# Optimization experiments

Hardware: AMD Instinct MI355X
Metric: run time of the kernel (lower is better)

The kernel has to match this reference:

```python
import jax, jax.numpy as jnp
import numpy as np

PIANO_SAMPLES = 2_621_440          # multiple of 256 (~119 s @ 22050 Hz)
BLOCK = 512
HOP = 256
N_STEPS = PIANO_SAMPLES // HOP      # 10240 loop iterations
N_FRAMES = PIANO_SAMPLES // HOP + 2 # 10242
UPSAMPLE = 256 // 32                # 8, as in F.upsample(scale_factor=8)


def _hamming(n=BLOCK):
    # torch.hamming_window default: periodic=True
    return (0.54 - 0.46 * jnp.cos(2.0 * jnp.pi * jnp.arange(n, dtype=jnp.float32) / n)).astype(jnp.float32)


def _upsample_linear(v, scale):
    # F.upsample(mode='linear', align_corners=False) on a 1D signal
    n = v.shape[0]
    coords = (jnp.arange(n * scale, dtype=jnp.float32) + 0.5) / scale - 0.5
    coords = jnp.clip(coords, 0.0, n - 1.0)
    lo = jnp.floor(coords).astype(jnp.int32)
    hi = jnp.minimum(lo + 1, n - 1)
    w = coords - lo.astype(jnp.float32)
    return v[lo] * (1.0 - w) + v[hi] * w


def setup_inputs() -> dict:
    key = jax.random.key(0)
    k1, k2, k3, k4, k5, k6 = jax.random.split(key, 6)
    return {
        "x": jnp.zeros((1,), jnp.float32),  # unused by the original forward
        "excitation_env": jax.random.uniform(k1, (N_FRAMES * 32,), jnp.float32) * 0.01,
        "tf_real": jax.random.uniform(k2, (N_FRAMES, 257), jnp.float32) * 0.2,
        "tf_imag": jax.random.uniform(k3, (N_FRAMES, 257), jnp.float32) * 0.2,
        "etf_real": jax.random.uniform(k4, (257,), jnp.float32) * 0.2,
        "etf_imag": jax.random.uniform(k5, (257,), jnp.float32) * 0.2,
        # per-step uniform(-1,1) noise (torch draws this inside forward)
        "noise": jax.random.uniform(k6, (N_STEPS, BLOCK), jnp.float32) * 2.0 - 1.0,
    }


def reference(x, excitation_env, tf_real, tf_imag, etf_real, etf_imag, noise):
    tf = (tf_real + 1j * tf_imag).astype(jnp.complex64)      # [N_FRAMES, 257]
    etf = (etf_real + 1j * etf_imag).astype(jnp.complex64)   # [257]
    win = _hamming()

    # excitation envelope: square then linear-upsample x8 -> len PIANO_SAMPLES + 512
    exc = _upsample_linear(excitation_env ** 2, UPSAMPLE)

    # gather all 512-sample excitation windows at hop 256 -> [N_STEPS, 512]
    idx = jnp.arange(N_STEPS)[:, None] * HOP + jnp.arange(BLOCK)[None, :]
    exc_blocks = exc[idx]

    # batched excitation filtering (independent per step -> fully vectorized)
    imp = noise * exc_blocks
    imp = jnp.fft.irfft(jnp.fft.rfft(imp, norm='ortho') * etf, norm='ortho').astype(jnp.float32)

    # impulse added to the *previous* block at steps 1..N_STEPS-1; last block gets none
    imp_next = jnp.concatenate([imp[1:], jnp.zeros((1, BLOCK), imp.dtype)], axis=0)

    def step(s, inp):
        tf_i, inext = inp
        b = win * jnp.fft.irfft(jnp.fft.rfft(s, norm='ortho') * tf_i, norm='ortho').astype(jnp.float32)
        s_next = b + inext
        return s_next, s_next

    s0 = imp[0]  # learned_impulse=False -> first block is the filtered excitation
    _, ys = jax.lax.scan(step, s0, (tf[:N_STEPS], imp_next))

    blocks = jnp.concatenate([s0[None, :], ys], axis=0)  # [N_STEPS+1, 512]

    # overlap-add with hop 256
    n_b = blocks.shape[0]
    out = jnp.zeros((n_b * HOP + (BLOCK - HOP),), blocks.dtype)
    oa_idx = jnp.arange(n_b)[:, None] * HOP + jnp.arange(BLOCK)[None, :]
    out = out.at[oa_idx].add(blocks)
    return out[:PIANO_SAMPLES]
```

## Files before the change

### kernel.cpp

```cpp
#include <hip/hip_runtime.h>
#include <math.h>

#define N_STEPS 10240
#define ROWF2 264
#define ROWF  (ROWF2*2)
#define SROWF 512
#define ENV_N 327744
#define LCH 16
#define KWARM 16

typedef float f4 __attribute__((ext_vector_type(4)));

__device__ inline float2 mkf2(float x, float y) { return make_float2(x, y); }

template<int DIR>
__device__ inline void waveFFT256(float2 v[4], const int l,
                                  const float Tc, const float Ts,
                                  const float ux, const float uy) {
  const int rb = (int)(__brev((unsigned)l) >> 26);
  #pragma unroll
  for (int r = 0; r < 4; ++r) {
    v[r].x = __shfl(v[r].x, rb);
    v[r].y = __shfl(v[r].y, rb);
  }
  #pragma unroll
  for (int s = 0; s < 6; ++s) {
    const int half = 1 << s;
    float wx, wy;
    if (s == 0) { wx = (l & 1) ? -1.f : 1.f; wy = 0.f; }
    else {
      const int idx = (l << (5 - s)) & 63;
      wx = __shfl(Tc, idx);
      float tsv = __shfl(Ts, idx);
      wy = (DIR < 0) ? tsv : -tsv;
    }
    #pragma unroll
    for (int r = 0; r < 4; ++r) {
      float tx = __shfl_xor(v[r].x, half);
      float ty = __shfl_xor(v[r].y, half);
      const bool low = (l & half) == 0;
      float ax = low ? v[r].x : tx, ay = low ? v[r].y : ty;
      float bx = low ? tx : v[r].x, by = low ? ty : v[r].y;
      v[r].x = ax + (wx * bx - wy * by);
      v[r].y = ay + (wx * by + wy * bx);
    }
  }
  const float u2x = ux * ux - uy * uy, u2y = 2.f * ux * uy;
  const float u3x = u2x * ux - u2y * uy, u3y = u2x * uy + u2y * ux;
  float2 t0 = v[0];
  float2 t1 = mkf2(v[1].x * ux - v[1].y * uy, v[1].x * uy + v[1].y * ux);
  float2 t2 = mkf2(v[2].x * u2x - v[2].y * u2y, v[2].x * u2y + v[2].y * u2x);
  float2 t3 = mkf2(v[3].x * u3x - v[3].y * u3y, v[3].x * u3y + v[3].y * u3x);
  float2 p02 = mkf2(t0.x + t2.x, t0.y + t2.y), m02 = mkf2(t0.x - t2.x, t0.y - t2.y);
  float2 p13 = mkf2(t1.x + t3.x, t1.y + t3.y), m13 = mkf2(t1.x - t3.x, t1.y - t3.y);
  v[0] = mkf2(p02.x + p13.x, p02.y + p13.y);
  v[2] = mkf2(p02.x - p13.x, p02.y - p13.y);
  if (DIR < 0) {
    v[1] = mkf2(m02.x + m13.y, m02.y - m13.x);
    v[3] = mkf2(m02.x - m13.y, m02.y + m13.x);
  } else {
    v[1] = mkf2(m02.x - m13.y, m02.y + m13.x);
    v[3] = mkf2(m02.x + m13.y, m02.y - m13.x);
  }
}

__global__ __launch_bounds__(256) void kernA(const float* __restrict__ env,
                                             const float* __restrict__ noise,
                                             const float* __restrict__ tf_re,
                                             const float* __restrict__ etf_re,
                                             const float* __restrict__ etf_im,
                                             float* __restrict__ IMP,
                                             float* __restrict__ T256,
                                             float* __restrict__ I256) {
  const int l = threadIdx.x & 63;
  const int j = blockIdx.x * 4 + (threadIdx.x >> 6);
  float* rowf = IMP + (size_t)j * ROWF;
  float2* row = (float2*)rowf;
  if (j >= N_STEPS) {
    if (j == N_STEPS) {
      #pragma unroll
      for (int r = 0; r < 4; ++r) row[64 * r + l] = mkf2(0.f, 0.f);
      if (l == 0) { row[256] = mkf2(0.f, 0.f); I256[N_STEPS] = 0.f; }
    }
    return;
  }
  const int K = 32 * j + l;
  float e0 = env[K];                e0 *= e0;
  float em = env[max(K - 1, 0)];    em *= em;
  float ep = env[min(K + 1, ENV_N - 1)]; ep *= ep;
  float sm[8];
  #pragma unroll
  for (int u = 0; u < 8; ++u) {
    float val;
    if (u < 4) {
      float fr = 0.5625f + 0.125f * (float)u;
      val = em * (1.f - fr) + e0 * fr;
      if (K == 0) val = e0;
    } else {
      float fr = 0.0625f + 0.125f * (float)(u - 4);
      val = e0 * (1.f - fr) + ep * fr;
    }
    sm[u] = val;
  }
  const float4* np = (const float4*)(noise + (size_t)j * 512 + 8 * l);
  float4 n0 = np[0], n1 = np[1];
  float nn[8] = {n0.x, n0.y, n0.z, n0.w, n1.x, n1.y, n1.z, n1.w};
  float2 v[4];
  #pragma unroll
  for (int r = 0; r < 4; ++r)
    v[r] = mkf2(nn[2 * r] * sm[2 * r], nn[2 * r + 1] * sm[2 * r + 1]);

  float ca, sa; sincosf(-0.01227184630308513f * (float)l, &sa, &ca);
  const float ux = ca * ca - sa * sa, uy = 2.f * ca * sa;
  float Tc, Ts; sincosf(-0.09817477042468103f * (float)l, &Ts, &Tc);

  waveFFT256<-1>(v, l, Tc, Ts, ux, uy);

  float2 Zc[4];
  const int pidx = (64 - l) & 63;
  #pragma unroll
  for (int r = 0; r < 4; ++r) {
    Zc[r].x = __shfl(v[3 - r].x, pidx);
    Zc[r].y = __shfl(v[3 - r].y, pidx);
  }
  float2 z0lane = v[0];
  if (l == 0) { Zc[0] = v[0]; Zc[1] = v[3]; Zc[2] = v[2]; Zc[3] = v[1]; }
  constexpr float crA[4] = {1.f, 0.7071067811865476f, 0.f, -0.7071067811865476f};
  constexpr float srA[4] = {0.f, -0.7071067811865476f, -1.f, -0.7071067811865476f};
  const float FS = 0.04419417382415922f;
  #pragma unroll
  for (int r = 0; r < 4; ++r) {
    float Ex = 0.5f * (v[r].x + Zc[r].x), Ey = 0.5f * (v[r].y - Zc[r].y);
    float Dx = v[r].x - Zc[r].x,          Dy = v[r].y + Zc[r].y;
    float Ox = 0.5f * Dy, Oy = -0.5f * Dx;
    float c  = crA[r] * ca - srA[r] * sa;
    float sn = crA[r] * sa + srA[r] * ca;
    float Wx = (Ex + (c * Ox - sn * Oy)) * FS;
    float Wy = (Ey + (c * Oy + sn * Ox)) * FS;
    int k = 64 * r + l;
    float er = etf_re[k], ei = etf_im[k];
    float Px = Wx * er - Wy * ei;
    float Py = Wx * ei + Wy * er;
    if (k == 0) Py = 0.f;
    row[k] = mkf2(Px, Py);
  }
  if (l == 0) {
    float W256 = (z0lane.x - z0lane.y) * FS;
    float imp256 = W256 * etf_re[256];
    row[256] = mkf2(imp256, 0.f);
    I256[j] = imp256;
    T256[j] = tf_re[(size_t)j * 257 + 256];
  }
}

struct Slot { f4 tr, ti, ia, ib; };

__device__ inline void issueSlot(Slot& b, int i, int l,
                                 const float* __restrict__ tf_re,
                                 const float* __restrict__ tf_im,
                                 const float* __restrict__ IMP) {
  const float* atr = tf_re + (size_t)i * 257 + 4 * l;
  const float* ati = tf_im + (size_t)i * 257 + 4 * l;
  const float* aim = IMP + (size_t)(i + 1) * ROWF + 8 * l;
  asm volatile("global_load_dwordx4 %0, %1, off" : "=v"(b.tr) : "v"(atr));
  asm volatile("global_load_dwordx4 %0, %1, off" : "=v"(b.ti) : "v"(ati));
  asm volatile("global_load_dwordx4 %0, %1, off" : "=v"(b.ia) : "v"(aim));
  asm volatile("global_load_dwordx4 %0, %1, off offset:16" : "=v"(b.ib) : "v"(aim));
}

__device__ inline void doStep(const Slot& b, int l, float tfr256, float imp256,
                              float2& s0, float2& s1, float2& s2, float2& s3,
                              float& s256) {
  float2 y0, y1, y2, y3;
  y0.x = s0.x * b.tr[0] - s0.y * b.ti[0];  y0.y = s0.x * b.ti[0] + s0.y * b.tr[0];
  y1.x = s1.x * b.tr[1] - s1.y * b.ti[1];  y1.y = s1.x * b.ti[1] + s1.y * b.tr[1];
  y2.x = s2.x * b.tr[2] - s2.y * b.ti[2];  y2.y = s2.x * b.ti[2] + s2.y * b.tr[2];
  y3.x = s3.x * b.tr[3] - s3.y * b.ti[3];  y3.y = s3.x * b.ti[3] + s3.y * b.tr[3];
  if (l == 0) y0.y = 0.f;
  float Y256 = tfr256 * s256;
  float phx = __shfl_up(y3.x, 1), phy = __shfl_up(y3.y, 1);
  float nlx = __shfl_down(y0.x, 1), nly = __shfl_down(y0.y, 1);
  float2 p0 = (l == 0)  ? mkf2(y1.x, -y1.y) : mkf2(phx, phy);
  float2 n3 = (l == 63) ? mkf2(Y256, 0.f)   : mkf2(nlx, nly);
  float y255x = __shfl(y3.x, 63);
  const float A = 0.54f, Bc = 0.23f;
  float2 c0, c1, c2, c3;
  c0.x = A * y0.x - Bc * (p0.x + y1.x);  c0.y = A * y0.y - Bc * (p0.y + y1.y);
  c1.x = A * y1.x - Bc * (y0.x + y2.x);  c1.y = A * y1.y - Bc * (y0.y + y2.y);
  c2.x = A * y2.x - Bc * (y1.x + y3.x);  c2.y = A * y2.y - Bc * (y1.y + y3.y);
  c3.x = A * y3.x - Bc * (y2.x + n3.x);  c3.y = A * y3.y - Bc * (y2.y + n3.y);
  float C256 = A * Y256 - 0.46f * y255x;
  s0.x = c0.x + b.ia[0];  s0.y = c0.y + b.ia[1];
  s1.x = c1.x + b.ia[2];  s1.y = c1.y + b.ia[3];
  s2.x = c2.x + b.ib[0];  s2.y = c2.y + b.ib[1];
  s3.x = c3.x + b.ib[2];  s3.y = c3.y + b.ib[3];
  s256 = C256 + imp256;
}

__global__ __launch_bounds__(64, 1) void kernB(const float* __restrict__ tf_re,
                                               const float* __restrict__ tf_im,
                                               const float* __restrict__ IMP,
                                               const float* __restrict__ T256,
                                               const float* __restrict__ I256,
                                               float* __restrict__ S,
                                               float* __restrict__ S256a) {
  const int c = blockIdx.x, l = threadIdx.x;
  const int j0 = c * LCH;
  const int w0 = (c > 0) ? (j0 - KWARM) : 0;
  const int WOFF = (c > 0) ? KWARM : 0;

  __shared__ float Ssh[LCH * SROWF];

  float t256v = T256[min(w0 + l, N_STEPS - 1)];
  float i256v = I256[min(w0 + 1 + l, N_STEPS)];

  float2 s0 = mkf2(0.f, 0.f), s1 = s0, s2 = s0, s3 = s0;
  float s256 = 0.f, s256keep = 0.f;

  if (c == 0) {
    const float4* r4 = (const float4*)IMP;
    float4 a = r4[2 * l], bb = r4[2 * l + 1];
    s0 = mkf2(a.x, a.y);  s1 = mkf2(a.z, a.w);
    s2 = mkf2(bb.x, bb.y); s3 = mkf2(bb.z, bb.w);
    s256 = IMP[512];
    float4* o4 = (float4*)S;
    o4[2 * l] = a; o4[2 * l + 1] = bb;
    if (l == 0) S256a[0] = s256;
  }

  asm volatile("" :: "v"(t256v), "v"(i256v));
  asm volatile("s_waitcnt vmcnt(0)" ::: "memory");

  Slot b0, b1, b2, b3, b4, b5, b6, b7;
  issueSlot(b0, w0 + 0, l, tf_re, tf_im, IMP);
  issueSlot(b1, w0 + 1, l, tf_re, tf_im, IMP);
  issueSlot(b2, w0 + 2, l, tf_re, tf_im, IMP);
  issueSlot(b3, w0 + 3, l, tf_re, tf_im, IMP);
  issueSlot(b4, w0 + 4, l, tf_re, tf_im, IMP);
  issueSlot(b5, w0 + 5, l, tf_re, tf_im, IMP);
  issueSlot(b6, w0 + 6, l, tf_re, tf_im, IMP);
  issueSlot(b7, w0 + 7, l, tf_re, tf_im, IMP);

  #define WAITN(NSTR) \
    asm volatile("s_waitcnt vmcnt(" NSTR ")" ::: "memory"); \
    __builtin_amdgcn_sched_barrier(0);

  #define WARMSTEP(BUF, M) { \
    WAITN("28") \
    const float tfr_ = __shfl(t256v, M); \
    const float im2_ = __shfl(i256v, M); \
    doStep(BUF, l, tfr_, im2_, s0, s1, s2, s3, s256); \
    issueSlot(BUF, w0 + (M) + 8, l, tf_re, tf_im, IMP); }

  #define SAVE_LDS(K) { \
    float4* d4 = (float4*)(Ssh + (K) * SROWF + 8 * l); \
    d4[0] = make_float4(s0.x, s0.y, s1.x, s1.y); \
    d4[1] = make_float4(s2.x, s2.y, s3.x, s3.y); \
    if (l == (K)) s256keep = s256; }

  #define MAINSTEP(BUF, K) { \
    WAITN("28") \
    const float tfr_ = __shfl(t256v, WOFF + (K)); \
    const float im2_ = __shfl(i256v, WOFF + (K)); \
    doStep(BUF, l, tfr_, im2_, s0, s1, s2, s3, s256); \
    SAVE_LDS(K) \
    issueSlot(BUF, j0 + (K) + 8, l, tf_re, tf_im, IMP); }

  #define MAINSTEPL(BUF, K, NSTR) { \
    WAITN(NSTR) \
    const float tfr_ = __shfl(t256v, WOFF + (K)); \
    const float im2_ = __shfl(i256v, WOFF + (K)); \
    doStep(BUF, l, tfr_, im2_, s0, s1, s2, s3, s256); \
    SAVE_LDS(K) }

  if (c > 0) {
    WARMSTEP(b0, 0)  WARMSTEP(b1, 1)  WARMSTEP(b2, 2)  WARMSTEP(b3, 3)
    WARMSTEP(b4, 4)  WARMSTEP(b5, 5)  WARMSTEP(b6, 6)  WARMSTEP(b7, 7)
    WARMSTEP(b0, 8)  WARMSTEP(b1, 9)  WARMSTEP(b2, 10) WARMSTEP(b3, 11)
    WARMSTEP(b4, 12) WARMSTEP(b5, 13) WARMSTEP(b6, 14) WARMSTEP(b7, 15)
  }

  MAINSTEP(b0, 0)  MAINSTEP(b1, 1)  MAINSTEP(b2, 2)  MAINSTEP(b3, 3)
  MAINSTEP(b4, 4)  MAINSTEP(b5, 5)  MAINSTEP(b6, 6)  MAINSTEP(b7, 7)
  MAINSTEPL(b0, 8,  "28") MAINSTEPL(b1, 9,  "24")
  MAINSTEPL(b2, 10, "20") MAINSTEPL(b3, 11, "16")
  MAINSTEPL(b4, 12, "12") MAINSTEPL(b5, 13, "8")
  MAINSTEPL(b6, 14, "4")  MAINSTEPL(b7, 15, "0")

  #undef WAITN
  #undef WARMSTEP
  #undef SAVE_LDS
  #undef MAINSTEP
  #undef MAINSTEPL

  for (int K = 0; K < LCH; ++K) {
    const float4* i4 = (const float4*)(Ssh + K * SROWF + 8 * l);
    float4* o4 = (float4*)(S + (size_t)(j0 + 1 + K) * SROWF + 8 * l);
    o4[0] = i4[0];
    o4[1] = i4[1];
  }
  if (l < LCH) S256a[j0 + 1 + l] = s256keep;
}

__global__ __launch_bounds__(576) void kernC(const float* __restrict__ S,
                                             const float* __restrict__ S256a,
                                             float* __restrict__ out) {
  const int l = threadIdx.x & 63;
  const int w = threadIdx.x >> 6;
  const int b = blockIdx.x;
  const int r = 8 * b - 1 + w;
  __shared__ float2 ybuf[9][256];
  if (r < 0) {
    #pragma unroll
    for (int rr = 0; rr < 4; ++rr) ybuf[0][64 * rr + l] = mkf2(0.f, 0.f);
  } else {
    const float4* r4 = (const float4*)(S + (size_t)r * SROWF);
    float4 a = r4[2 * l], bb = r4[2 * l + 1];
    float2 W[4] = {mkf2(a.x, a.y), mkf2(a.z, a.w), mkf2(bb.x, bb.y), mkf2(bb.z, bb.w)};
    float w256 = S256a[r];
    float2 Wm[4];
    const int pidx = (64 - l) & 63;
    Wm[0].x = __shfl(W[0].x, pidx);
    Wm[0].y = __shfl(W[0].y, pidx);
    if (l == 0) Wm[0] = mkf2(w256, 0.f);
    Wm[1].x = __shfl_xor(W[3].x, 63);  Wm[1].y = __shfl_xor(W[3].y, 63);
    Wm[2].x = __shfl_xor(W[2].x, 63);  Wm[2].y = __shfl_xor(W[2].y, 63);
    Wm[3].x = __shfl_xor(W[1].x, 63);  Wm[3].y = __shfl_xor(W[1].y, 63);
    float cu, su; sincosf(0.02454369260617026f * (float)l, &su, &cu);
    const float cl = cu * cu - su * su, sl_ = 2.f * cu * su;
    float Tc, Ts; sincosf(-0.09817477042468103f * (float)l, &Ts, &Tc);
    constexpr float crC[4] = {1.f, 0.9999247018391445f, 0.9996988186962042f, 0.9993223845883495f};
    constexpr float srC[4] = {0.f, 0.0122715382857199f, 0.0245412285229123f, 0.0368072229413588f};
    float2 v[4];
    #pragma unroll
    for (int rr = 0; rr < 4; ++rr) {
      float Ex = 0.5f * (W[rr].x + Wm[rr].x), Ey = 0.5f * (W[rr].y - Wm[rr].y);
      float Dx = W[rr].x - Wm[rr].x,          Dy = W[rr].y + Wm[rr].y;
      float c  = cl * crC[rr] - sl_ * srC[rr];
      float sn = cl * srC[rr] + sl_ * crC[rr];
      float Ox = 0.5f * (c * Dx - sn * Dy);
      float Oy = 0.5f * (c * Dy + sn * Dx);
      v[rr] = mkf2(Ex - Oy, Ey + Ox);
    }
    waveFFT256<+1>(v, l, Tc, Ts, cu, su);
    const float ISC = 0.08838834764831845f;
    #pragma unroll
    for (int rr = 0; rr < 4; ++rr)
      ybuf[w][64 * rr + l] = mkf2(v[rr].x * ISC, v[rr].y * ISC);
  }
  __syncthreads();
  float2* out2 = (float2*)out;
  const size_t base = (size_t)b * 1024;
  for (int idx = threadIdx.x; idx < 1024; idx += 576) {
    const int k = idx >> 7, t2 = idx & 127;
    float2 a = ybuf[k + 1][t2];
    float2 p = ybuf[k][128 + t2];
    out2[base + idx] = mkf2(a.x + p.x, a.y + p.y);
  }
}

extern "C" void kernel_launch(void* const* d_in, const int* in_sizes, int n_in,
                              void* d_out, int out_size, void* d_ws, size_t ws_size,
                              hipStream_t stream) {
  const float* env    = (const float*)d_in[1];
  const float* tf_re  = (const float*)d_in[2];
  const float* tf_im  = (const float*)d_in[3];
  const float* etf_re = (const float*)d_in[4];
  const float* etf_im = (const float*)d_in[5];
  const float* noise  = (const float*)d_in[6];
  float* out = (float*)d_out;

  float* wsf = (float*)d_ws;
  float* IMP   = wsf;
  float* S     = wsf + (size_t)(N_STEPS + 1) * ROWF;
  float* T256  = S + (size_t)(N_STEPS + 1) * SROWF;
  float* I256  = T256 + N_STEPS;
  float* S256a = I256 + (N_STEPS + 1);

  kernA<<<(N_STEPS / 4) + 1, 256, 0, stream>>>(env, noise, tf_re, etf_re, etf_im,
                                               IMP, T256, I256);
  kernB<<<N_STEPS / LCH, 64, 0, stream>>>(tf_re, tf_im, IMP, T256, I256, S, S256a);
  kernC<<<N_STEPS / 8, 576, 0, stream>>>(S, S256a, out);
}
```

Measured before the change: 54.83 us.

## Replace rolling register prefetch in scan kernel with bulk LDS staging bursts

The chunked recurrence kernel no longer keeps an 8-deep ring of inline-asm global loads with hand-tuned vmcnt waits. It now loads all 16 steps' transfer-function and impulse rows into shared memory in one burst per phase, then consumes them from LDS, reusing the impulse buffer to hold the saved states. The launch bound's single-block occupancy hint is also dropped. This aims for simpler code and more loads in flight at once, but it serialises load and compute phases and adds LDS round-trips on every step.

```diff
diff --git a/kernel.cpp b/kernel.cpp
--- a/kernel.cpp
+++ b/kernel.cpp
@@ -9,7 +9,8 @@
 #define LCH 16
 #define KWARM 16
 
-typedef float f4 __attribute__((ext_vector_type(4)));
+typedef float f4  __attribute__((ext_vector_type(4)));
+typedef float f4a __attribute__((ext_vector_type(4), aligned(4)));
 
 __device__ inline float2 mkf2(float x, float y) { return make_float2(x, y); }
 
@@ -153,29 +154,16 @@
   }
 }
 
-struct Slot { f4 tr, ti, ia, ib; };
-
-__device__ inline void issueSlot(Slot& b, int i, int l,
-                                 const float* __restrict__ tf_re,
-                                 const float* __restrict__ tf_im,
-                                 const float* __restrict__ IMP) {
-  const float* atr = tf_re + (size_t)i * 257 + 4 * l;
-  const float* ati = tf_im + (size_t)i * 257 + 4 * l;
-  const float* aim = IMP + (size_t)(i + 1) * ROWF + 8 * l;
-  asm volatile("global_load_dwordx4 %0, %1, off" : "=v"(b.tr) : "v"(atr));
-  asm volatile("global_load_dwordx4 %0, %1, off" : "=v"(b.ti) : "v"(ati));
-  asm volatile("global_load_dwordx4 %0, %1, off" : "=v"(b.ia) : "v"(aim));
-  asm volatile("global_load_dwordx4 %0, %1, off offset:16" : "=v"(b.ib) : "v"(aim));
-}
-
-__device__ inline void doStep(const Slot& b, int l, float tfr256, float imp256,
+__device__ inline void doStep(const f4& tr, const f4& ti,
+                              const float4& ia, const float4& ib,
+                              int l, float tfr256, float imp256,
                               float2& s0, float2& s1, float2& s2, float2& s3,
                               float& s256) {
   float2 y0, y1, y2, y3;
-  y0.x = s0.x * b.tr[0] - s0.y * b.ti[0];  y0.y = s0.x * b.ti[0] + s0.y * b.tr[0];
-  y1.x = s1.x * b.tr[1] - s1.y * b.ti[1];  y1.y = s1.x * b.ti[1] + s1.y * b.tr[1];
-  y2.x = s2.x * b.tr[2] - s2.y * b.ti[2];  y2.y = s2.x * b.ti[2] + s2.y * b.tr[2];
-  y3.x = s3.x * b.tr[3] - s3.y * b.ti[3];  y3.y = s3.x * b.ti[3] + s3.y * b.tr[3];
+  y0.x = s0.x * tr[0] - s0.y * ti[0];  y0.y = s0.x * ti[0] + s0.y * tr[0];
+  y1.x = s1.x * tr[1] - s1.y * ti[1];  y1.y = s1.x * ti[1] + s1.y * tr[1];
+  y2.x = s2.x * tr[2] - s2.y * ti[2];  y2.y = s2.x * ti[2] + s2.y * tr[2];
+  y3.x = s3.x * tr[3] - s3.y * ti[3];  y3.y = s3.x * ti[3] + s3.y * tr[3];
   if (l == 0) y0.y = 0.f;
   float Y256 = tfr256 * s256;
   float phx = __shfl_up(y3.x, 1), phy = __shfl_up(y3.y, 1);
@@ -190,26 +178,28 @@
   c2.x = A * y2.x - Bc * (y1.x + y3.x);  c2.y = A * y2.y - Bc * (y1.y + y3.y);
   c3.x = A * y3.x - Bc * (y2.x + n3.x);  c3.y = A * y3.y - Bc * (y2.y + n3.y);
   float C256 = A * Y256 - 0.46f * y255x;
-  s0.x = c0.x + b.ia[0];  s0.y = c0.y + b.ia[1];
-  s1.x = c1.x + b.ia[2];  s1.y = c1.y + b.ia[3];
-  s2.x = c2.x + b.ib[0];  s2.y = c2.y + b.ib[1];
-  s3.x = c3.x + b.ib[2];  s3.y = c3.y + b.ib[3];
+  s0.x = c0.x + ia.x;  s0.y = c0.y + ia.y;
+  s1.x = c1.x + ia.z;  s1.y = c1.y + ia.w;
+  s2.x = c2.x + ib.x;  s2.y = c2.y + ib.y;
+  s3.x = c3.x + ib.z;  s3.y = c3.y + ib.w;
   s256 = C256 + imp256;
 }
 
-__global__ __launch_bounds__(64, 1) void kernB(const float* __restrict__ tf_re,
-                                               const float* __restrict__ tf_im,
-                                               const float* __restrict__ IMP,
-                                               const float* __restrict__ T256,
-                                               const float* __restrict__ I256,
-                                               float* __restrict__ S,
-                                               float* __restrict__ S256a) {
+__global__ __launch_bounds__(64) void kernB(const float* __restrict__ tf_re,
+                                            const float* __restrict__ tf_im,
+                                            const float* __restrict__ IMP,
+                                            const float* __restrict__ T256,
+                                            const float* __restrict__ I256,
+                                            float* __restrict__ S,
+                                            float* __restrict__ S256a) {
   const int c = blockIdx.x, l = threadIdx.x;
   const int j0 = c * LCH;
-  const int w0 = (c > 0) ? (j0 - KWARM) : 0;
+  const int w0 = (c > 0) ? (j0 - KWARM) : j0;
   const int WOFF = (c > 0) ? KWARM : 0;
 
-  __shared__ float Ssh[LCH * SROWF];
+  __shared__ float4 TFRE[16][64];
+  __shared__ float4 TFIM[16][64];
+  __shared__ float4 IMRW[16][128];
 
   float t256v = T256[min(w0 + l, N_STEPS - 1)];
   float i256v = I256[min(w0 + 1 + l, N_STEPS)];
@@ -228,76 +218,50 @@
     if (l == 0) S256a[0] = s256;
   }
 
-  asm volatile("" :: "v"(t256v), "v"(i256v));
-  asm volatile("s_waitcnt vmcnt(0)" ::: "memory");
-
-  Slot b0, b1, b2, b3, b4, b5, b6, b7;
-  issueSlot(b0, w0 + 0, l, tf_re, tf_im, IMP);
-  issueSlot(b1, w0 + 1, l, tf_re, tf_im, IMP);
-  issueSlot(b2, w0 + 2, l, tf_re, tf_im, IMP);
-  issueSlot(b3, w0 + 3, l, tf_re, tf_im, IMP);
-  issueSlot(b4, w0 + 4, l, tf_re, tf_im, IMP);
-  issueSlot(b5, w0 + 5, l, tf_re, tf_im, IMP);
-  issueSlot(b6, w0 + 6, l, tf_re, tf_im, IMP);
-  issueSlot(b7, w0 + 7, l, tf_re, tf_im, IMP);
-
-  #define WAITN(NSTR) \
-    asm volatile("s_waitcnt vmcnt(" NSTR ")" ::: "memory"); \
-    __builtin_amdgcn_sched_barrier(0);
-
-  #define WARMSTEP(BUF, M) { \
-    WAITN("28") \
-    const float tfr_ = __shfl(t256v, M); \
-    const float im2_ = __shfl(i256v, M); \
-    doStep(BUF, l, tfr_, im2_, s0, s1, s2, s3, s256); \
-    issueSlot(BUF, w0 + (M) + 8, l, tf_re, tf_im, IMP); }
-
-  #define SAVE_LDS(K) { \
-    float4* d4 = (float4*)(Ssh + (K) * SROWF + 8 * l); \
-    d4[0] = make_float4(s0.x, s0.y, s1.x, s1.y); \
-    d4[1] = make_float4(s2.x, s2.y, s3.x, s3.y); \
-    if (l == (K)) s256keep = s256; }
-
-  #define MAINSTEP(BUF, K) { \
-    WAITN("28") \
-    const float tfr_ = __shfl(t256v, WOFF + (K)); \
-    const float im2_ = __shfl(i256v, WOFF + (K)); \
-    doStep(BUF, l, tfr_, im2_, s0, s1, s2, s3, s256); \
-    SAVE_LDS(K) \
-    issueSlot(BUF, j0 + (K) + 8, l, tf_re, tf_im, IMP); }
-
-  #define MAINSTEPL(BUF, K, NSTR) { \
-    WAITN(NSTR) \
-    const float tfr_ = __shfl(t256v, WOFF + (K)); \
-    const float im2_ = __shfl(i256v, WOFF + (K)); \
-    doStep(BUF, l, tfr_, im2_, s0, s1, s2, s3, s256); \
-    SAVE_LDS(K) }
+  #define BURST(base) { \
+    _Pragma("unroll") \
+    for (int k = 0; k < 16; ++k) { \
+      const int i = (base) + k; \
+      f4a vr = *(const f4a*)(tf_re + (size_t)i * 257 + 4 * l); \
+      f4a vi = *(const f4a*)(tf_im + (size_t)i * 257 + 4 * l); \
+      TFRE[k][l] = make_float4(vr[0], vr[1], vr[2], vr[3]); \
+      TFIM[k][l] = make_float4(vi[0], vi[1], vi[2], vi[3]); \
+      const float4* ims = (const float4*)(IMP + (size_t)(i + 1) * ROWF); \
+      IMRW[k][2 * l]     = ims[2 * l]; \
+      IMRW[k][2 * l + 1] = ims[2 * l + 1]; \
+    } }
+
+  #define CONSUME(boff, SAVE) { \
+    for (int k = 0; k < 16; ++k) { \
+      float4 trf = TFRE[k][l], tif = TFIM[k][l]; \
+      f4 tr, ti; \
+      tr[0] = trf.x; tr[1] = trf.y; tr[2] = trf.z; tr[3] = trf.w; \
+      ti[0] = tif.x; ti[1] = tif.y; ti[2] = tif.z; ti[3] = tif.w; \
+      float4 ia = IMRW[k][2 * l], ib = IMRW[k][2 * l + 1]; \
+      const float tfr_ = __shfl(t256v, (boff) + k); \
+      const float im2_ = __shfl(i256v, (boff) + k); \
+      doStep(tr, ti, ia, ib, l, tfr_, im2_, s0, s1, s2, s3, s256); \
+      if (SAVE) { \
+        IMRW[k][2 * l]     = make_float4(s0.x, s0.y, s1.x, s1.y); \
+        IMRW[k][2 * l + 1] = make_float4(s2.x, s2.y, s3.x, s3.y); \
+        if (l == k) s256keep = s256; \
+      } \
+    } }
 
   if (c > 0) {
-    WARMSTEP(b0, 0)  WARMSTEP(b1, 1)  WARMSTEP(b2, 2)  WARMSTEP(b3, 3)
-    WARMSTEP(b4, 4)  WARMSTEP(b5, 5)  WARMSTEP(b6, 6)  WARMSTEP(b7, 7)
-    WARMSTEP(b0, 8)  WARMSTEP(b1, 9)  WARMSTEP(b2, 10) WARMSTEP(b3, 11)
-    WARMSTEP(b4, 12) WARMSTEP(b5, 13) WARMSTEP(b6, 14) WARMSTEP(b7, 15)
-  }
-
-  MAINSTEP(b0, 0)  MAINSTEP(b1, 1)  MAINSTEP(b2, 2)  MAINSTEP(b3, 3)
-  MAINSTEP(b4, 4)  MAINSTEP(b5, 5)  MAINSTEP(b6, 6)  MAINSTEP(b7, 7)
-  MAINSTEPL(b0, 8,  "28") MAINSTEPL(b1, 9,  "24")
-  MAINSTEPL(b2, 10, "20") MAINSTEPL(b3, 11, "16")
-  MAINSTEPL(b4, 12, "12") MAINSTEPL(b5, 13, "8")
-  MAINSTEPL(b6, 14, "4")  MAINSTEPL(b7, 15, "0")
-
-  #undef WAITN
-  #undef WARMSTEP
-  #undef SAVE_LDS
-  #undef MAINSTEP
-  #undef MAINSTEPL
-
-  for (int K = 0; K < LCH; ++K) {
-    const float4* i4 = (const float4*)(Ssh + K * SROWF + 8 * l);
-    float4* o4 = (float4*)(S + (size_t)(j0 + 1 + K) * SROWF + 8 * l);
-    o4[0] = i4[0];
-    o4[1] = i4[1];
+    BURST(w0)
+    CONSUME(0, false)
+  }
+  BURST(j0)
+  CONSUME(WOFF, true)
+
+  #undef BURST
+  #undef CONSUME
+
+  for (int k = 0; k < 16; ++k) {
+    float4* o4 = (float4*)(S + (size_t)(j0 + 1 + k) * SROWF + 8 * l);
+    o4[0] = IMRW[k][2 * l];
+    o4[1] = IMRW[k][2 * l + 1];
   }
   if (l < LCH) S256a[j0 + 1 + l] = s256keep;
 }
```

New measurement: 81.75 us. 49.1% more time.
